# Performance work log

Hardware: AMD Instinct MI355X
Metric: run time of the kernel (lower is better)

## Reference

```python
import jax, jax.numpy as jnp
import numpy as np

B, S, H, E, I, TOP_K = 2, 1024, 1024, 8, 1408, 2
W_SCALE = 0.02


def setup_inputs() -> dict:
    key = jax.random.key(0)
    ks = jax.random.split(key, 5)
    return {
        "hidden_states": jax.random.normal(ks[0], (B, S, H), dtype=jnp.float32),
        "router_weight": jax.random.normal(ks[1], (H, E), dtype=jnp.float32) * W_SCALE,
        "gate_proj": jax.random.normal(ks[2], (E, H, I), dtype=jnp.float32) * W_SCALE,
        "up_proj": jax.random.normal(ks[3], (E, H, I), dtype=jnp.float32) * W_SCALE,
        "down_proj": jax.random.normal(ks[4], (E, I, H), dtype=jnp.float32) * W_SCALE,
        "gate_bias": jnp.zeros((E, I), dtype=jnp.float32),
        "up_bias": jnp.zeros((E, I), dtype=jnp.float32),
        "down_bias": jnp.zeros((E, H), dtype=jnp.float32),
        "top_k": TOP_K,
    }


def reference(hidden_states, router_weight, gate_proj, up_proj, down_proj,
              gate_bias, up_bias, down_bias, top_k):
    b, s, h = hidden_states.shape
    e = gate_proj.shape[0]
    x = hidden_states.reshape(-1, h)              # [T, H], T = b*s
    t = x.shape[0]

    # --- RouterAdapter: MoEGate top-k then scatter into dense scores [T, E] ---
    logits = x @ router_weight                    # [T, E]
    probs = jax.nn.softmax(logits, axis=-1)
    topk_w, topk_idx = jax.lax.top_k(probs, top_k)  # [T, k]
    topk_w = topk_w / jnp.sum(topk_w, axis=-1, keepdims=True)  # norm_topk_prob
    scores = jnp.zeros((t, e), dtype=topk_w.dtype)
    scores = scores.at[jnp.arange(t)[:, None], topk_idx].set(topk_w)

    # --- StackedExperts.sparse_forward (dense equivalent of sparse matmuls) ---
    g = jnp.einsum('th,ehi->tei', x, gate_proj) + gate_bias[None]  # [T, E, I]
    u = jnp.einsum('th,ehi->tei', x, up_proj) + up_bias[None]      # [T, E, I]
    act = jax.nn.silu(g) * u                       # ACTIVATION_DEEPSEEK
    d = jnp.einsum('tei,eih->teh', act, down_proj) + down_bias[None]  # [T, E, H]

    # combine per-expert outputs with router scores (non-routed scores are 0,
    # matching the sparse matmul's zero blocks)
    y = jnp.einsum('teh,te->th', d, scores)
    return y.reshape(b, s, h)
```

## Files before the change

kernel.cpp:

```cpp
#include <hip/hip_runtime.h>

#define T_TOK 2048
#define HDIM  1024
#define NEXP  8
#define IDIM  1408

#define BM 128
#define BN 64
#define BK 32
#define KPAD 40
#define MT_SLOTS 16
#define GU_NT 22
#define DN_NT 16
#define DK_HALF 704

typedef __attribute__((ext_vector_type(8))) short bf16x8;
typedef __attribute__((ext_vector_type(4))) float f32x4;

static __device__ __forceinline__ unsigned short f2bf(float f) {
    union { float f; unsigned u; } a; a.f = f;
    return (unsigned short)((a.u + 0x7fffu + ((a.u >> 16) & 1u)) >> 16);
}

__global__ __launch_bounds__(256) void router_compute_kernel(
    const float* __restrict__ x,
    const float* __restrict__ rw,
    int*   __restrict__ sel,
    float* __restrict__ w1arr,
    unsigned short* __restrict__ xb)
{
    __shared__ float rwT[NEXP][HDIM];
    const int tid = threadIdx.x;
#pragma unroll
    for (int p = 0; p < 4; ++p) {
        const int h = tid + 256 * p;
        const float4 a = *(const float4*)(rw + (size_t)h * 8);
        const float4 b = *(const float4*)(rw + (size_t)h * 8 + 4);
        rwT[0][h] = a.x; rwT[1][h] = a.y; rwT[2][h] = a.z; rwT[3][h] = a.w;
        rwT[4][h] = b.x; rwT[5][h] = b.y; rwT[6][h] = b.z; rwT[7][h] = b.w;
    }
    __syncthreads();

    const int wave = (blockIdx.x * blockDim.x + threadIdx.x) >> 6;
    const int lane = threadIdx.x & 63;
    if (wave >= T_TOK) return;
    const int t = wave;

    float xr[16];
    const float* xp = x + (size_t)t * HDIM;
#pragma unroll
    for (int i = 0; i < 16; ++i) xr[i] = xp[lane + 64 * i];

    unsigned short* xbp = xb + (size_t)t * HDIM;
#pragma unroll
    for (int i = 0; i < 16; ++i) xbp[lane + 64 * i] = f2bf(xr[i]);

    double logits[NEXP];
#pragma unroll
    for (int e = 0; e < NEXP; ++e) {
        double s = 0.0;
#pragma unroll
        for (int i = 0; i < 16; ++i)
            s += (double)xr[i] * (double)rwT[e][lane + 64 * i];
#pragma unroll
        for (int off = 32; off > 0; off >>= 1)
            s += __shfl_down(s, off, 64);
        logits[e] = s;
    }

    if (lane == 0) {
        int e1 = 0;
        for (int e = 1; e < NEXP; ++e) if (logits[e] > logits[e1]) e1 = e;
        int e2 = -1;
        for (int e = 0; e < NEXP; ++e) {
            if (e == e1) continue;
            if (e2 < 0 || logits[e] > logits[e2]) e2 = e;
        }
        const double w1 = 1.0 / (1.0 + exp(logits[e2] - logits[e1]));
        sel[t]   = e1 | (e2 << 8);
        w1arr[t] = (float)w1;
    }
}

__global__ __launch_bounds__(1024) void router_scatter_kernel(
    const int* __restrict__ sel, const float* __restrict__ w1arr,
    int* __restrict__ counts,
    int* __restrict__ tok_list, float* __restrict__ wgt_list,
    int* __restrict__ row_list)
{
    __shared__ int cnt[NEXP];
    const int tid = threadIdx.x;
    if (tid < NEXP) cnt[tid] = 0;
    __syncthreads();
    for (int t = tid; t < T_TOK; t += 1024) {
        const int s  = sel[t];
        const int e1 = s & 255, e2 = s >> 8;
        const float w1 = w1arr[t];
        const int p1 = atomicAdd(&cnt[e1], 1);
        tok_list[e1 * T_TOK + p1] = t;
        wgt_list[e1 * T_TOK + p1] = w1;
        row_list[e1 * T_TOK + p1] = 2 * t;
        const int p2 = atomicAdd(&cnt[e2], 1);
        tok_list[e2 * T_TOK + p2] = t;
        wgt_list[e2 * T_TOK + p2] = 1.0f - w1;
        row_list[e2 * T_TOK + p2] = 2 * t + 1;
    }
    __syncthreads();
    if (tid < NEXP) counts[tid] = cnt[tid];
}

__global__ __launch_bounds__(256) void wtrans_all_kernel(
    const float* __restrict__ gw, const float* __restrict__ uw,
    const float* __restrict__ dw,
    unsigned short* __restrict__ gwt, unsigned short* __restrict__ uwt,
    unsigned short* __restrict__ dwt)
{
    const int z  = blockIdx.z;
    const int bx = blockIdx.x;
    const float* src; unsigned short* dst; int K, N, kb, nb;
    if (z < 16) {
        K = HDIM; N = IDIM;
        const int e = z & 7;
        src = (z < 8 ? gw : uw) + (size_t)e * K * N;
        dst = (z < 8 ? gwt : uwt) + (size_t)e * (size_t)N * K;
        nb = bx % 11; kb = bx / 11;
    } else {
        K = IDIM; N = HDIM;
        const int e = z - 16;
        src = dw + (size_t)e * K * N;
        dst = dwt + (size_t)e * (size_t)N * K;
        nb = bx & 7; kb = bx >> 3;
    }

    const int tid  = threadIdx.x;
    const int wv   = tid >> 6;
    const int lane = tid & 63;
    const int k0 = kb * 64 + (wv >> 1) * 32 + (lane >> 4) * 8;
    const int n0 = nb * 128 + (wv & 1) * 64 + (lane & 15) * 4;

    float4 v[8];
#pragma unroll
    for (int r = 0; r < 8; ++r)
        v[r] = *(const float4*)(src + (size_t)(k0 + r) * N + n0);

#pragma unroll
    for (int i = 0; i < 4; ++i) {
        ushort4 lo, hi;
        lo.x = f2bf(((const float*)&v[0])[i]);
        lo.y = f2bf(((const float*)&v[1])[i]);
        lo.z = f2bf(((const float*)&v[2])[i]);
        lo.w = f2bf(((const float*)&v[3])[i]);
        hi.x = f2bf(((const float*)&v[4])[i]);
        hi.y = f2bf(((const float*)&v[5])[i]);
        hi.z = f2bf(((const float*)&v[6])[i]);
        hi.w = f2bf(((const float*)&v[7])[i]);
        unsigned short* dp = dst + (size_t)(n0 + i) * K + k0;
        *(ushort4*)(dp)     = lo;
        *(ushort4*)(dp + 4) = hi;
    }
}

__global__ __launch_bounds__(256) void gateup_kernel(
    const unsigned short* __restrict__ xb,
    const unsigned short* __restrict__ gwt,
    const unsigned short* __restrict__ uwt,
    const float* __restrict__ gb, const float* __restrict__ ub,
    const int* __restrict__ counts,
    const int* __restrict__ tok_list,
    const int* __restrict__ row_list,
    unsigned short* __restrict__ act)
{
    const int flat = blockIdx.x;
    const int xcd  = flat & 7;
    const int q    = flat >> 3;
    const int mt   = q & 15;
    const int slot = q >> 4;
    const int P    = slot * 8 + xcd;
    const int e    = P / GU_NT;
    const int nt   = P % GU_NT;
    const int n_e  = counts[e];
    const int m0   = mt * BM;
    if (m0 >= n_e) return;
    const int n0 = nt * BN;

    const unsigned short* gwp = gwt + (size_t)e * IDIM * HDIM;
    const unsigned short* uwp = uwt + (size_t)e * IDIM * HDIM;
    const float* gbp = gb + (size_t)e * IDIM;
    const float* ubp = ub + (size_t)e * IDIM;

    __shared__ unsigned short As[BM][KPAD];
    __shared__ unsigned short Bg[BN][KPAD];
    __shared__ unsigned short Bu[BN][KPAD];
    __shared__ int gr_lds[BM];
    __shared__ int or_lds[BM];

    const int tid = threadIdx.x;
    const int base = e * T_TOK;
    if (tid < BM) {
        const int m = m0 + tid;
        int g = -1, o = -1;
        if (m < n_e) { g = tok_list[base + m]; o = row_list[base + m]; }
        gr_lds[tid] = g; or_lds[tid] = o;
    }
    __syncthreads();

    const int ar = tid >> 1;
    const int ac = (tid & 1) * 16;
    const int arow = gr_lds[ar];
    const unsigned short* ap = xb + (size_t)(arow < 0 ? 0 : arow) * HDIM;
    const int u   = tid & 127;
    const int brow = u >> 1;
    const int bch  = (u & 1) * 16;
    const unsigned short* bsrc =
        ((tid >> 7) ? uwp : gwp) + (size_t)(n0 + brow) * HDIM + bch;
    unsigned short* Bdst =
        ((tid >> 7) ? &Bu[0][0] : &Bg[0][0]) + brow * KPAD + bch;

    const int wv = tid >> 6, lane = tid & 63;
    const int wm = (wv & 1) * 64, wn = (wv >> 1) * 32;
    const int l16 = lane & 15, quad = lane >> 4;

    f32x4 accg[4][2], accu[4][2];
    const f32x4 zero = {0.0f, 0.0f, 0.0f, 0.0f};
#pragma unroll
    for (int i = 0; i < 4; ++i)
#pragma unroll
        for (int j = 0; j < 2; ++j) { accg[i][j] = zero; accu[i][j] = zero; }

    uint4 PA0 = {0,0,0,0}, PA1 = {0,0,0,0}, PB0, PB1;
    if (arow >= 0) {
        PA0 = *(const uint4*)(ap + ac);
        PA1 = *(const uint4*)(ap + ac + 8);
    }
    PB0 = *(const uint4*)(bsrc);
    PB1 = *(const uint4*)(bsrc + 8);

    for (int k0 = 0; k0 < HDIM; k0 += BK) {
        __syncthreads();
        *(uint4*)&As[ar][ac]       = PA0;
        *(uint4*)&As[ar][ac + 8]   = PA1;
        *(uint4*)(Bdst)            = PB0;
        *(uint4*)(Bdst + 8)        = PB1;
        __syncthreads();

        const int kn = k0 + BK;
        if (kn < HDIM) {
            if (arow >= 0) {
                PA0 = *(const uint4*)(ap + kn + ac);
                PA1 = *(const uint4*)(ap + kn + ac + 8);
            }
            PB0 = *(const uint4*)(bsrc + kn);
            PB1 = *(const uint4*)(bsrc + kn + 8);
        }

        bf16x8 af[4], bgf[2], buf[2];
#pragma unroll
        for (int i = 0; i < 4; ++i)
            af[i] = *(const bf16x8*)&As[wm + i * 16 + l16][quad * 8];
#pragma unroll
        for (int j = 0; j < 2; ++j) {
            bgf[j] = *(const bf16x8*)&Bg[wn + j * 16 + l16][quad * 8];
            buf[j] = *(const bf16x8*)&Bu[wn + j * 16 + l16][quad * 8];
        }
#pragma unroll
        for (int i = 0; i < 4; ++i)
#pragma unroll
            for (int j = 0; j < 2; ++j) {
                accg[i][j] = __builtin_amdgcn_mfma_f32_16x16x32_bf16(
                    af[i], bgf[j], accg[i][j], 0, 0, 0);
                accu[i][j] = __builtin_amdgcn_mfma_f32_16x16x32_bf16(
                    af[i], buf[j], accu[i][j], 0, 0, 0);
            }
    }

#pragma unroll
    for (int j = 0; j < 2; ++j) {
        const int nl = n0 + wn + j * 16 + l16;
        const float gbv = gbp[nl];
        const float ubv = ubp[nl];
#pragma unroll
        for (int i = 0; i < 4; ++i) {
#pragma unroll
            for (int ii = 0; ii < 4; ++ii) {
                const int ml = wm + i * 16 + quad * 4 + ii;
                const int orow = or_lds[ml];
                if (orow >= 0) {
                    const float g = accg[i][j][ii] + gbv;
                    const float uu = accu[i][j][ii] + ubv;
                    act[(size_t)orow * IDIM + nl] =
                        f2bf(g * uu / (1.0f + __expf(-g)));
                }
            }
        }
    }
}

__global__ __launch_bounds__(256) void down_kernel(
    const unsigned short* __restrict__ act,
    const unsigned short* __restrict__ dwt,
    const float* __restrict__ db,
    const int* __restrict__ counts,
    const float* __restrict__ wgt_list,
    const int* __restrict__ row_list,
    float* __restrict__ y2)
{
    const int flat = blockIdx.x;
    const int xcd  = flat & 7;
    const int q    = flat >> 3;
    const int mt   = q & 15;
    const int slot = q >> 4;
    const int P    = slot * 8 + xcd;
    const int sk   = P & 1;
    const int en   = P >> 1;
    const int e    = en >> 4;
    const int nt   = en & 15;
    const int n_e  = counts[e];
    const int m0   = mt * BM;
    if (m0 >= n_e) return;
    const int n0 = nt * BN;
    const int ks = sk * DK_HALF;
    float* y2s = y2 + (size_t)sk * 2 * T_TOK * HDIM;

    const unsigned short* dwp = dwt + (size_t)e * HDIM * IDIM;
    const float* dbp = db + (size_t)e * HDIM;

    __shared__ unsigned short As[BM][KPAD];
    __shared__ unsigned short Bs[BN][KPAD];
    __shared__ int   r_lds[BM];
    __shared__ float w_lds[BM];

    const int tid = threadIdx.x;
    const int base = e * T_TOK;
    if (tid < BM) {
        const int m = m0 + tid;
        int r = -1; float w = 0.0f;
        if (m < n_e) { r = row_list[base + m]; w = wgt_list[base + m]; }
        r_lds[tid] = r; w_lds[tid] = w;
    }
    __syncthreads();

    const int ar = tid >> 1;
    const int ac = (tid & 1) * 16;
    const int arow = r_lds[ar];
    const unsigned short* ap = act + (size_t)(arow < 0 ? 0 : arow) * IDIM + ks;
    const int brow = tid >> 2;
    const int bch  = (tid & 3) * 8;
    const unsigned short* bsrc = dwp + (size_t)(n0 + brow) * IDIM + ks + bch;
    unsigned short* Bdst = &Bs[0][0] + brow * KPAD + bch;

    const int wv = tid >> 6, lane = tid & 63;
    const int wm = (wv & 1) * 64, wn = (wv >> 1) * 32;
    const int l16 = lane & 15, quad = lane >> 4;

    f32x4 acc[4][2];
    const f32x4 zero = {0.0f, 0.0f, 0.0f, 0.0f};
#pragma unroll
    for (int i = 0; i < 4; ++i)
#pragma unroll
        for (int j = 0; j < 2; ++j) acc[i][j] = zero;

    uint4 PA0 = {0,0,0,0}, PA1 = {0,0,0,0}, PB;
    if (arow >= 0) {
        PA0 = *(const uint4*)(ap + ac);
        PA1 = *(const uint4*)(ap + ac + 8);
    }
    PB = *(const uint4*)(bsrc);

    for (int k0 = 0; k0 < DK_HALF; k0 += BK) {
        __syncthreads();
        *(uint4*)&As[ar][ac]     = PA0;
        *(uint4*)&As[ar][ac + 8] = PA1;
        *(uint4*)(Bdst)          = PB;
        __syncthreads();

        const int kn = k0 + BK;
        if (kn < DK_HALF) {
            if (arow >= 0) {
                PA0 = *(const uint4*)(ap + kn + ac);
                PA1 = *(const uint4*)(ap + kn + ac + 8);
            }
            PB = *(const uint4*)(bsrc + kn);
        }

        bf16x8 af[4], bfr[2];
#pragma unroll
        for (int i = 0; i < 4; ++i)
            af[i] = *(const bf16x8*)&As[wm + i * 16 + l16][quad * 8];
#pragma unroll
        for (int j = 0; j < 2; ++j)
            bfr[j] = *(const bf16x8*)&Bs[wn + j * 16 + l16][quad * 8];
#pragma unroll
        for (int i = 0; i < 4; ++i)
#pragma unroll
            for (int j = 0; j < 2; ++j)
                acc[i][j] = __builtin_amdgcn_mfma_f32_16x16x32_bf16(
                    af[i], bfr[j], acc[i][j], 0, 0, 0);
    }

#pragma unroll
    for (int j = 0; j < 2; ++j) {
        const int nl = n0 + wn + j * 16 + l16;
        const float bv = (sk == 0) ? dbp[nl] : 0.0f;
#pragma unroll
        for (int i = 0; i < 4; ++i) {
#pragma unroll
            for (int ii = 0; ii < 4; ++ii) {
                const int ml = wm + i * 16 + quad * 4 + ii;
                const int rr = r_lds[ml];
                if (rr >= 0)
                    y2s[(size_t)rr * HDIM + nl] = w_lds[ml] * (acc[i][j][ii] + bv);
            }
        }
    }
}

__global__ __launch_bounds__(256) void combine_kernel(
    const float* __restrict__ y2, float* __restrict__ out)
{
    const int idx = (blockIdx.x * 256 + threadIdx.x) * 4;
    const int t = idx >> 10;
    const int h = idx & 1023;
    const float* y2b = y2 + (size_t)2 * T_TOK * HDIM;
    const float4 a0 = *(const float4*)(y2  + ((size_t)2 * t) * HDIM + h);
    const float4 a1 = *(const float4*)(y2  + ((size_t)2 * t + 1) * HDIM + h);
    const float4 b0 = *(const float4*)(y2b + ((size_t)2 * t) * HDIM + h);
    const float4 b1 = *(const float4*)(y2b + ((size_t)2 * t + 1) * HDIM + h);
    float4 o;
    o.x = a0.x + a1.x + b0.x + b1.x;
    o.y = a0.y + a1.y + b0.y + b1.y;
    o.z = a0.z + a1.z + b0.z + b1.z;
    o.w = a0.w + a1.w + b0.w + b1.w;
    *(float4*)(out + idx) = o;
}

extern "C" void kernel_launch(void* const* d_in, const int* in_sizes, int n_in,
                              void* d_out, int out_size, void* d_ws, size_t ws_size,
                              hipStream_t stream)
{
    const float* x      = (const float*)d_in[0];
    const float* rw     = (const float*)d_in[1];
    const float* gate_w = (const float*)d_in[2];
    const float* up_w   = (const float*)d_in[3];
    const float* down_w = (const float*)d_in[4];
    const float* gate_b = (const float*)d_in[5];
    const float* up_b   = (const float*)d_in[6];
    const float* down_b = (const float*)d_in[7];
    float* out = (float*)d_out;

    char* ws = (char*)d_ws;
    size_t off = 0;
    int*   counts   = (int*)(ws + off);  off += 256;
    int*   tok_list = (int*)(ws + off);  off += 65536;
    float* wgt_list = (float*)(ws + off); off += 65536;
    int*   row_list = (int*)(ws + off);  off += 65536;
    int*   sel      = (int*)(ws + off);  off += T_TOK * 4;
    float* w1arr    = (float*)(ws + off); off += T_TOK * 4;
    unsigned short* x_bf = (unsigned short*)(ws + off); off += (size_t)T_TOK * HDIM * 2;
    unsigned short* act  = (unsigned short*)(ws + off); off += (size_t)2 * T_TOK * IDIM * 2;
    unsigned short* dwt  = (unsigned short*)(ws + off); off += (size_t)NEXP * IDIM * HDIM * 2;
    unsigned short* gwt  = (unsigned short*)(ws + off); off += (size_t)NEXP * IDIM * HDIM * 2;
    unsigned short* uwt  = (unsigned short*)(ws + off);
    float* y2 = (float*)gwt;

    wtrans_all_kernel<<<dim3(176, 1, 24), 256, 0, stream>>>(
        gate_w, up_w, down_w, gwt, uwt, dwt);

    router_compute_kernel<<<T_TOK / 4, 256, 0, stream>>>(x, rw, sel, w1arr, x_bf);

    router_scatter_kernel<<<1, 1024, 0, stream>>>(
        sel, w1arr, counts, tok_list, wgt_list, row_list);

    gateup_kernel<<<8 * GU_NT * MT_SLOTS, 256, 0, stream>>>(
        x_bf, gwt, uwt, gate_b, up_b, counts, tok_list, row_list, act);

    down_kernel<<<2 * 8 * DN_NT * MT_SLOTS, 256, 0, stream>>>(
        act, dwt, down_b, counts, wgt_list, row_list, y2);

    combine_kernel<<<(T_TOK * HDIM / 4) / 256, 256, 0, stream>>>(y2, out);
}
```

Baseline: 288.4 us.

## Fuse router with gate/up weight transpose and overlap down-weight transpose with gateup

Merges the router compute and the gate/up weight bf16 transpose into one prep kernel. The down-projection weight transpose now runs as extra blocks inside the gate/up GEMM launch, so it overlaps with the GEMM instead of running beforehand. The transpose itself now stages through an LDS tile so both global reads and writes are coalesced 16-byte accesses. This removes kernel launches and the serialized transpose time, but the LDS staging uses 2-byte column writes that may hit bank conflicts, and the GEMM blocks now share the GPU with transpose blocks.

```diff
diff --git a/kernel.cpp b/kernel.cpp
--- a/kernel.cpp
+++ b/kernel.cpp
@@ -14,6 +14,11 @@
 #define DN_NT 16
 #define DK_HALF 704
 
+#define GU_BLOCKS   (8 * GU_NT * MT_SLOTS)
+#define PREP_RTR    512
+#define PREP_GRID   (PREP_RTR + 16 * 176)
+#define GUWD_GRID   (GU_BLOCKS + 8 * 176)
+
 typedef __attribute__((ext_vector_type(8))) short bf16x8;
 typedef __attribute__((ext_vector_type(4))) float f32x4;
 
@@ -22,63 +27,108 @@
     return (unsigned short)((a.u + 0x7fffu + ((a.u >> 16) & 1u)) >> 16);
 }
 
-__global__ __launch_bounds__(256) void router_compute_kernel(
+__global__ __launch_bounds__(256) void prep_kernel(
     const float* __restrict__ x,
     const float* __restrict__ rw,
+    const float* __restrict__ gw,
+    const float* __restrict__ uw,
     int*   __restrict__ sel,
     float* __restrict__ w1arr,
-    unsigned short* __restrict__ xb)
+    unsigned short* __restrict__ xb,
+    unsigned short* __restrict__ gwt,
+    unsigned short* __restrict__ uwt)
 {
-    __shared__ float rwT[NEXP][HDIM];
+    __shared__ __align__(16) char smem[32768];
     const int tid = threadIdx.x;
-#pragma unroll
-    for (int p = 0; p < 4; ++p) {
-        const int h = tid + 256 * p;
-        const float4 a = *(const float4*)(rw + (size_t)h * 8);
-        const float4 b = *(const float4*)(rw + (size_t)h * 8 + 4);
-        rwT[0][h] = a.x; rwT[1][h] = a.y; rwT[2][h] = a.z; rwT[3][h] = a.w;
-        rwT[4][h] = b.x; rwT[5][h] = b.y; rwT[6][h] = b.z; rwT[7][h] = b.w;
-    }
-    __syncthreads();
-
-    const int wave = (blockIdx.x * blockDim.x + threadIdx.x) >> 6;
-    const int lane = threadIdx.x & 63;
-    if (wave >= T_TOK) return;
-    const int t = wave;
-
-    float xr[16];
-    const float* xp = x + (size_t)t * HDIM;
-#pragma unroll
-    for (int i = 0; i < 16; ++i) xr[i] = xp[lane + 64 * i];
-
-    unsigned short* xbp = xb + (size_t)t * HDIM;
-#pragma unroll
-    for (int i = 0; i < 16; ++i) xbp[lane + 64 * i] = f2bf(xr[i]);
-
-    double logits[NEXP];
-#pragma unroll
-    for (int e = 0; e < NEXP; ++e) {
-        double s = 0.0;
-#pragma unroll
-        for (int i = 0; i < 16; ++i)
-            s += (double)xr[i] * (double)rwT[e][lane + 64 * i];
-#pragma unroll
-        for (int off = 32; off > 0; off >>= 1)
-            s += __shfl_down(s, off, 64);
-        logits[e] = s;
-    }
-
-    if (lane == 0) {
-        int e1 = 0;
-        for (int e = 1; e < NEXP; ++e) if (logits[e] > logits[e1]) e1 = e;
-        int e2 = -1;
+    const int bx  = blockIdx.x;
+
+    if (bx < PREP_RTR) {
+        float (*rwT)[HDIM] = (float (*)[HDIM])smem;
+#pragma unroll
+        for (int p = 0; p < 4; ++p) {
+            const int h = tid + 256 * p;
+            const float4 a = *(const float4*)(rw + (size_t)h * 8);
+            const float4 b = *(const float4*)(rw + (size_t)h * 8 + 4);
+            rwT[0][h] = a.x; rwT[1][h] = a.y; rwT[2][h] = a.z; rwT[3][h] = a.w;
+            rwT[4][h] = b.x; rwT[5][h] = b.y; rwT[6][h] = b.z; rwT[7][h] = b.w;
+        }
+        __syncthreads();
+
+        const int t    = bx * 4 + (tid >> 6);
+        const int lane = tid & 63;
+        if (t >= T_TOK) return;
+
+        float xr[16];
+        const float* xp = x + (size_t)t * HDIM;
+#pragma unroll
+        for (int i = 0; i < 16; ++i) xr[i] = xp[lane + 64 * i];
+
+        unsigned short* xbp = xb + (size_t)t * HDIM;
+#pragma unroll
+        for (int i = 0; i < 16; ++i) xbp[lane + 64 * i] = f2bf(xr[i]);
+
+        double logits[NEXP];
+#pragma unroll
         for (int e = 0; e < NEXP; ++e) {
-            if (e == e1) continue;
-            if (e2 < 0 || logits[e] > logits[e2]) e2 = e;
-        }
-        const double w1 = 1.0 / (1.0 + exp(logits[e2] - logits[e1]));
-        sel[t]   = e1 | (e2 << 8);
-        w1arr[t] = (float)w1;
+            double s = 0.0;
+#pragma unroll
+            for (int i = 0; i < 16; ++i)
+                s += (double)xr[i] * (double)rwT[e][lane + 64 * i];
+#pragma unroll
+            for (int off = 32; off > 0; off >>= 1)
+                s += __shfl_down(s, off, 64);
+            logits[e] = s;
+        }
+
+        if (lane == 0) {
+            int e1 = 0;
+            for (int e = 1; e < NEXP; ++e) if (logits[e] > logits[e1]) e1 = e;
+            int e2 = -1;
+            for (int e = 0; e < NEXP; ++e) {
+                if (e == e1) continue;
+                if (e2 < 0 || logits[e] > logits[e2]) e2 = e;
+            }
+            const double w1 = 1.0 / (1.0 + exp(logits[e2] - logits[e1]));
+            sel[t]   = e1 | (e2 << 8);
+            w1arr[t] = (float)w1;
+        }
+    } else {
+        const int idx = bx - PREP_RTR;
+        const int z   = idx / 176;
+        const int b   = idx - z * 176;
+        const int e   = z & 7;
+        const float* src = (z < 8 ? gw : uw) + (size_t)e * HDIM * IDIM;
+        unsigned short* dst =
+            (z < 8 ? gwt : uwt) + (size_t)e * (size_t)IDIM * HDIM;
+        const int nb = b % 11, kb = b / 11;
+        const int k0 = kb * 64, n0 = nb * 128;
+
+        unsigned short (*tb)[66] = (unsigned short (*)[66])smem;
+
+        const int lk = tid >> 5;
+        const int ln = (tid & 31) * 4;
+#pragma unroll
+        for (int r = 0; r < 8; ++r) {
+            const int k = r * 8 + lk;
+            const float4 v =
+                *(const float4*)(src + (size_t)(k0 + k) * IDIM + n0 + ln);
+            tb[ln + 0][k] = f2bf(v.x);
+            tb[ln + 1][k] = f2bf(v.y);
+            tb[ln + 2][k] = f2bf(v.z);
+            tb[ln + 3][k] = f2bf(v.w);
+        }
+        __syncthreads();
+
+        const int wn = tid >> 3;
+        const int wk = (tid & 7) * 8;
+#pragma unroll
+        for (int p = 0; p < 4; ++p) {
+            const int n = p * 32 + wn;
+            const unsigned* rp = (const unsigned*)&tb[n][wk];
+            uint4 o;
+            o.x = rp[0]; o.y = rp[1]; o.z = rp[2]; o.w = rp[3];
+            *(uint4*)(dst + (size_t)(n0 + n) * HDIM + k0 + wk) = o;
+        }
     }
 }
 
@@ -109,58 +159,7 @@
     if (tid < NEXP) counts[tid] = cnt[tid];
 }
 
-__global__ __launch_bounds__(256) void wtrans_all_kernel(
-    const float* __restrict__ gw, const float* __restrict__ uw,
-    const float* __restrict__ dw,
-    unsigned short* __restrict__ gwt, unsigned short* __restrict__ uwt,
-    unsigned short* __restrict__ dwt)
-{
-    const int z  = blockIdx.z;
-    const int bx = blockIdx.x;
-    const float* src; unsigned short* dst; int K, N, kb, nb;
-    if (z < 16) {
-        K = HDIM; N = IDIM;
-        const int e = z & 7;
-        src = (z < 8 ? gw : uw) + (size_t)e * K * N;
-        dst = (z < 8 ? gwt : uwt) + (size_t)e * (size_t)N * K;
-        nb = bx % 11; kb = bx / 11;
-    } else {
-        K = IDIM; N = HDIM;
-        const int e = z - 16;
-        src = dw + (size_t)e * K * N;
-        dst = dwt + (size_t)e * (size_t)N * K;
-        nb = bx & 7; kb = bx >> 3;
-    }
-
-    const int tid  = threadIdx.x;
-    const int wv   = tid >> 6;
-    const int lane = tid & 63;
-    const int k0 = kb * 64 + (wv >> 1) * 32 + (lane >> 4) * 8;
-    const int n0 = nb * 128 + (wv & 1) * 64 + (lane & 15) * 4;
-
-    float4 v[8];
-#pragma unroll
-    for (int r = 0; r < 8; ++r)
-        v[r] = *(const float4*)(src + (size_t)(k0 + r) * N + n0);
-
-#pragma unroll
-    for (int i = 0; i < 4; ++i) {
-        ushort4 lo, hi;
-        lo.x = f2bf(((const float*)&v[0])[i]);
-        lo.y = f2bf(((const float*)&v[1])[i]);
-        lo.z = f2bf(((const float*)&v[2])[i]);
-        lo.w = f2bf(((const float*)&v[3])[i]);
-        hi.x = f2bf(((const float*)&v[4])[i]);
-        hi.y = f2bf(((const float*)&v[5])[i]);
-        hi.z = f2bf(((const float*)&v[6])[i]);
-        hi.w = f2bf(((const float*)&v[7])[i]);
-        unsigned short* dp = dst + (size_t)(n0 + i) * K + k0;
-        *(ushort4*)(dp)     = lo;
-        *(ushort4*)(dp + 4) = hi;
-    }
-}
-
-__global__ __launch_bounds__(256) void gateup_kernel(
+__global__ __launch_bounds__(256) void gateup_wd_kernel(
     const unsigned short* __restrict__ xb,
     const unsigned short* __restrict__ gwt,
     const unsigned short* __restrict__ uwt,
@@ -168,9 +167,58 @@
     const int* __restrict__ counts,
     const int* __restrict__ tok_list,
     const int* __restrict__ row_list,
-    unsigned short* __restrict__ act)
+    unsigned short* __restrict__ act,
+    const float* __restrict__ dw,
+    unsigned short* __restrict__ dwt)
 {
+    __shared__ __align__(16) char smem[21504];
+    const int tid  = threadIdx.x;
     const int flat = blockIdx.x;
+
+    if (flat >= GU_BLOCKS) {
+        const int idx = flat - GU_BLOCKS;
+        const int e   = idx / 176;
+        const int b   = idx - e * 176;
+        const float* src = dw + (size_t)e * IDIM * HDIM;
+        unsigned short* dst = dwt + (size_t)e * (size_t)HDIM * IDIM;
+        const int nb = b & 7, kb = b >> 3;
+        const int k0 = kb * 64, n0 = nb * 128;
+
+        unsigned short (*tb)[66] = (unsigned short (*)[66])smem;
+
+        const int lk = tid >> 5;
+        const int ln = (tid & 31) * 4;
+#pragma unroll
+        for (int r = 0; r < 8; ++r) {
+            const int k = r * 8 + lk;
+            const float4 v =
+                *(const float4*)(src + (size_t)(k0 + k) * HDIM + n0 + ln);
+            tb[ln + 0][k] = f2bf(v.x);
+            tb[ln + 1][k] = f2bf(v.y);
+            tb[ln + 2][k] = f2bf(v.z);
+            tb[ln + 3][k] = f2bf(v.w);
+        }
+        __syncthreads();
+
+        const int wn = tid >> 3;
+        const int wk = (tid & 7) * 8;
+#pragma unroll
+        for (int p = 0; p < 4; ++p) {
+            const int n = p * 32 + wn;
+            const unsigned* rp = (const unsigned*)&tb[n][wk];
+            uint4 o;
+            o.x = rp[0]; o.y = rp[1]; o.z = rp[2]; o.w = rp[3];
+            *(uint4*)(dst + (size_t)(n0 + n) * IDIM + k0 + wk) = o;
+        }
+        return;
+    }
+
+    unsigned short (*As)[KPAD] = (unsigned short (*)[KPAD])smem;
+    unsigned short (*Bg)[KPAD] = (unsigned short (*)[KPAD])(smem + 10240);
+    unsigned short (*Bu)[KPAD] = (unsigned short (*)[KPAD])(smem + 15360);
+    int* gr_lds = (int*)(smem + 20480);
+    int* or_lds = (int*)(smem + 20992);
+
     const int xcd  = flat & 7;
     const int q    = flat >> 3;
     const int mt   = q & 15;
@@ -188,13 +236,6 @@
     const float* gbp = gb + (size_t)e * IDIM;
     const float* ubp = ub + (size_t)e * IDIM;
 
-    __shared__ unsigned short As[BM][KPAD];
-    __shared__ unsigned short Bg[BN][KPAD];
-    __shared__ unsigned short Bu[BN][KPAD];
-    __shared__ int gr_lds[BM];
-    __shared__ int or_lds[BM];
-
-    const int tid = threadIdx.x;
     const int base = e * T_TOK;
     if (tid < BM) {
         const int m = m0 + tid;
@@ -253,14 +294,14 @@
             PB1 = *(const uint4*)(bsrc + kn + 8);
         }
 
-        bf16x8 af[4], bgf[2], buf[2];
+        bf16x8 af[4], bgf[2], buf_[2];
 #pragma unroll
         for (int i = 0; i < 4; ++i)
             af[i] = *(const bf16x8*)&As[wm + i * 16 + l16][quad * 8];
 #pragma unroll
         for (int j = 0; j < 2; ++j) {
-            bgf[j] = *(const bf16x8*)&Bg[wn + j * 16 + l16][quad * 8];
-            buf[j] = *(const bf16x8*)&Bu[wn + j * 16 + l16][quad * 8];
+            bgf[j]  = *(const bf16x8*)&Bg[wn + j * 16 + l16][quad * 8];
+            buf_[j] = *(const bf16x8*)&Bu[wn + j * 16 + l16][quad * 8];
         }
 #pragma unroll
         for (int i = 0; i < 4; ++i)
@@ -269,7 +310,7 @@
                 accg[i][j] = __builtin_amdgcn_mfma_f32_16x16x32_bf16(
                     af[i], bgf[j], accg[i][j], 0, 0, 0);
                 accu[i][j] = __builtin_amdgcn_mfma_f32_16x16x32_bf16(
-                    af[i], buf[j], accu[i][j], 0, 0, 0);
+                    af[i], buf_[j], accu[i][j], 0, 0, 0);
             }
     }
 
@@ -462,16 +503,15 @@
     unsigned short* uwt  = (unsigned short*)(ws + off);
     float* y2 = (float*)gwt;
 
-    wtrans_all_kernel<<<dim3(176, 1, 24), 256, 0, stream>>>(
-        gate_w, up_w, down_w, gwt, uwt, dwt);
-
-    router_compute_kernel<<<T_TOK / 4, 256, 0, stream>>>(x, rw, sel, w1arr, x_bf);
+    prep_kernel<<<PREP_GRID, 256, 0, stream>>>(
+        x, rw, gate_w, up_w, sel, w1arr, x_bf, gwt, uwt);
 
     router_scatter_kernel<<<1, 1024, 0, stream>>>(
         sel, w1arr, counts, tok_list, wgt_list, row_list);
 
-    gateup_kernel<<<8 * GU_NT * MT_SLOTS, 256, 0, stream>>>(
-        x_bf, gwt, uwt, gate_b, up_b, counts, tok_list, row_list, act);
+    gateup_wd_kernel<<<GUWD_GRID, 256, 0, stream>>>(
+        x_bf, gwt, uwt, gate_b, up_b, counts, tok_list, row_list, act,
+        down_w, dwt);
 
     down_kernel<<<2 * 8 * DN_NT * MT_SLOTS, 256, 0, stream>>>(
         act, dwt, down_b, counts, wgt_list, row_list, y2);
```

Result: faster. 277.5 us (-3.8%).
